# Kernel tuning notes

Measured on AMD Instinct MI355X. Metric: run time of the kernel, lower is better.

The kernel has to match this reference:

```python
import jax, jax.numpy as jnp
import numpy as np

PCH_SIZE = 8
STRIDE = 3


def setup_inputs() -> dict:
    key = jax.random.key(0)
    x = jax.random.normal(key, (8, 3, 512, 512), dtype=jnp.float32)
    return {"x": x}


def _estimate_noise(x, p=PCH_SIZE, s=STRIDE):
    B = x.shape[0]
    # Extract overlapping patches: [B, C*p*p, Hp, Wp] (NCHW input).
    pch = jax.lax.conv_general_dilated_patches(x, (p, p), (s, s), 'VALID')
    d = pch.shape[1]                       # C*p*p = 192
    pch = pch.reshape(B, d, -1)            # [B, d, num_pch]
    num_pch = pch.shape[-1]
    mu = pch.mean(axis=-1, keepdims=True)
    X = pch - mu
    # Patch covariance: [B, d, d]
    sigma_X = jnp.einsum('bdn,ben->bde', X, X) / num_pch
    sig = jnp.sort(jnp.linalg.eigvalsh(sigma_X), axis=-1)  # [B, d], ascending

    # Vectorized version of the original sequential threshold search.
    # Loop iteration ii = -1..-d uses prefix sig[..., :d+ii] of length L = d-1..0.
    ks = jnp.arange(d)
    L = d - 1 - ks                          # prefix lengths in original loop order
    csum = jnp.cumsum(sig, axis=-1)         # [B, d]
    prefix_sum = jnp.where(L > 0, csum[:, jnp.clip(L - 1, 0, d - 1)], 0.0)  # [B, d]
    tau = prefix_sum / jnp.maximum(L, 1).astype(sig.dtype)                  # [B, d]

    j = jnp.arange(d)
    in_prefix = j[None, :] < L[:, None]     # [K, d] membership of eig j in prefix k
    greater = (sig[:, None, :] > tau[:, :, None]) & in_prefix[None]
    less = (sig[:, None, :] < tau[:, :, None]) & in_prefix[None]
    valid = greater.sum(axis=-1) == less.sum(axis=-1)  # [B, K]

    # First valid iteration in loop order (mirrors the `found` flag).
    idx = jnp.argmax(valid, axis=-1)                    # [B]
    tau_sel = jnp.take_along_axis(tau, idx[:, None], axis=-1)[:, 0]
    return jnp.sqrt(tau_sel)                             # [B]


def reference(x):
    return _estimate_noise(x)
```

## Files before the change

kernel.cpp:

```cpp
#include <hip/hip_runtime.h>
#include <math.h>

#define NB 8
#define NC 3
#define PD 192
#define IMG 512
#define NP 169
#define NPATCH 28561
#define INV_N (1.0f/28561.0f)
#define KST 32

typedef float f4 __attribute__((ext_vector_type(4)));
typedef f4 f4u __attribute__((aligned(4)));
typedef __bf16 bf16x8 __attribute__((ext_vector_type(8)));
typedef float f32x4 __attribute__((ext_vector_type(4)));

__device__ __forceinline__ float rdlane(float v, int lane) {
  return __uint_as_float(__builtin_amdgcn_readlane(__float_as_uint(v), lane));
}

template<int CTRL, int RM, int BM>
__device__ __forceinline__ float dpp_add(float x) {
  int sh = __builtin_amdgcn_update_dpp(0, __float_as_int(x), CTRL, RM, BM, false);
  return x + __int_as_float(sh);
}
__device__ __forceinline__ float wave_sum(float x) {
  x = dpp_add<0x111, 0xF, 0xF>(x);
  x = dpp_add<0x112, 0xF, 0xF>(x);
  x = dpp_add<0x114, 0xF, 0xF>(x);
  x = dpp_add<0x118, 0xF, 0xF>(x);
  x = dpp_add<0x142, 0xA, 0xF>(x);
  x = dpp_add<0x143, 0xC, 0xF>(x);
  return rdlane(x, 63);
}
__device__ __forceinline__ float row16_sum(float x) {
  x = dpp_add<0x111, 0xF, 0xF>(x);
  x = dpp_add<0x112, 0xF, 0xF>(x);
  x = dpp_add<0x114, 0xF, 0xF>(x);
  x = dpp_add<0x118, 0xF, 0xF>(x);
  return rdlane(x, 15);
}

__device__ __forceinline__ unsigned bfh(float v) {
  unsigned u = __float_as_uint(v);
  return (u + 0x7FFFu + ((u >> 16) & 1u)) >> 16;
}

__global__ __launch_bounds__(256) void row_sums_k(const float* __restrict__ x,
                                                  float* __restrict__ S) {
  int bid = blockIdx.x;
  int b = bid / PD, d = bid - b * PD;
  int c = d >> 6, ii = (d >> 3) & 7, jj = d & 7;
  const float* img = x + ((size_t)(b * NC + c)) * (IMG * IMG);
  float part = 0.f;
  for (int p = threadIdx.x; p < NPATCH; p += 256) {
    int ph = p / NP;
    int pw = p - ph * NP;
    part += img[(3 * ph + ii) * IMG + 3 * pw + jj];
  }
  __shared__ float red[256];
  int t = threadIdx.x;
  red[t] = part; __syncthreads();
  for (int s = 128; s > 0; s >>= 1) { if (t < s) red[t] += red[t + s]; __syncthreads(); }
  if (t == 0) S[bid] = red[0];
}

__global__ __launch_bounds__(512) void cov_gemm_k(const float* __restrict__ x,
                                                  float* __restrict__ partial,
                                                  int CH, int chunkSize) {
  int chunk = blockIdx.x % CH;
  int b = blockIdx.x / CH;
  int p0 = chunk * chunkSize;
  int pcount = NPATCH - p0;
  if (pcount > chunkSize) pcount = chunkSize;
  if (pcount < 0) pcount = 0;
  int nkt = (pcount + KST - 1) / KST;
  int pend = p0 + pcount;

  __shared__ unsigned short hiT[PD * 40];
  __shared__ unsigned short loT[PD * 40];

  int t = threadIdx.x;
  int l = t & 63, w = t >> 6;
  int wr = w >> 2, wc = w & 3;
  int m0 = wr * 96, n0 = wc * 48;
  const float* imgb = x + (size_t)b * NC * IMG * IMG;

  f32x4 acc[6][3];
#pragma unroll
  for (int i = 0; i < 6; ++i)
#pragma unroll
    for (int j = 0; j < 3; ++j)
      acc[i][j] = (f32x4){0.f, 0.f, 0.f, 0.f};

  int krow = (l >> 4) << 3;
  int rsel = l & 15;

  for (int kt = 0; kt < nkt; ++kt) {
    int pbase = p0 + kt * KST;
#pragma unroll
    for (int s = 0; s < 6; ++s) {
      int idx = (s << 9) + t;
      int f = idx >> 4, p2 = idx & 15;
      int c = f >> 6, ii = (f >> 3) & 7, jj = f & 7;
      const float* imgc = imgb + (size_t)c * IMG * IMG;
      int P0 = pbase + (p2 << 1);
      float v0 = 0.f, v1 = 0.f;
      if (P0 < pend) { int ph = P0 / NP, pw = P0 - ph * NP; v0 = imgc[(3 * ph + ii) * IMG + 3 * pw + jj]; }
      if (P0 + 1 < pend) { int ph = (P0 + 1) / NP, pw = (P0 + 1) - ph * NP; v1 = imgc[(3 * ph + ii) * IMG + 3 * pw + jj]; }
      unsigned h0 = bfh(v0), h1 = bfh(v1);
      float r0 = v0 - __uint_as_float(h0 << 16);
      float r1 = v1 - __uint_as_float(h1 << 16);
      unsigned g0 = bfh(r0), g1 = bfh(r1);
      *(unsigned*)&hiT[f * 40 + (p2 << 1)] = h0 | (h1 << 16);
      *(unsigned*)&loT[f * 40 + (p2 << 1)] = g0 | (g1 << 16);
    }
    __syncthreads();

    bf16x8 ah[6], al[6], bh[3], bl[3];
#pragma unroll
    for (int i = 0; i < 6; ++i) {
      int row = m0 + i * 16 + rsel;
      ah[i] = *(const bf16x8*)&hiT[row * 40 + krow];
      al[i] = *(const bf16x8*)&loT[row * 40 + krow];
    }
#pragma unroll
    for (int j = 0; j < 3; ++j) {
      int row = n0 + j * 16 + rsel;
      bh[j] = *(const bf16x8*)&hiT[row * 40 + krow];
      bl[j] = *(const bf16x8*)&loT[row * 40 + krow];
    }
#pragma unroll
    for (int i = 0; i < 6; ++i)
#pragma unroll
      for (int j = 0; j < 3; ++j) {
        acc[i][j] = __builtin_amdgcn_mfma_f32_16x16x32_bf16(ah[i], bh[j], acc[i][j], 0, 0, 0);
        acc[i][j] = __builtin_amdgcn_mfma_f32_16x16x32_bf16(ah[i], bl[j], acc[i][j], 0, 0, 0);
        acc[i][j] = __builtin_amdgcn_mfma_f32_16x16x32_bf16(al[i], bh[j], acc[i][j], 0, 0, 0);
      }
    __syncthreads();
  }

  float* outp = partial + ((size_t)chunk * NB + b) * PD * PD;
#pragma unroll
  for (int i = 0; i < 6; ++i) {
    int rowb = m0 + i * 16 + ((l >> 4) << 2);
#pragma unroll
    for (int r = 0; r < 4; ++r)
#pragma unroll
      for (int j = 0; j < 3; ++j)
        outp[(size_t)(rowb + r) * PD + n0 + j * 16 + (l & 15)] = acc[i][j][r];
  }
}

__global__ __launch_bounds__(256) void reduce_fin_k(const float* __restrict__ partial,
                                                    const float* __restrict__ S,
                                                    float* __restrict__ G, int CH) {
  int e = blockIdx.x * 256 + threadIdx.x;
  const int tot = NB * PD * PD;
  if (e >= tot) return;
  int b = e / (PD * PD);
  int rem = e - b * PD * PD;
  int i = rem / PD, j = rem - i * PD;
  float s = 0.f;
  for (int c = 0; c < CH; ++c) s += partial[((size_t)c * NB + b) * PD * PD + rem];
  float mui = S[b * PD + i] * INV_N, muj = S[b * PD + j] * INV_N;
  G[e] = s * INV_N - mui * muj;
}

__global__ __launch_bounds__(768, 3) void eigen_k(const float* __restrict__ sigma,
                                                  float* __restrict__ out) {
  __shared__ float ppt[PD][20];
  __shared__ float vvg[2][PD];
  __shared__ float wvg[PD];
  __shared__ float red0[2];
  __shared__ float red2[16];
  __shared__ float dd[PD], ee[PD], e2[PD];
  __shared__ float sig[PD], csum[PD];
  __shared__ float grd[8];
  __shared__ float scanw[4];
  __shared__ int   redi[4];
  __shared__ int   cntb[4][PD];

  int b = blockIdx.x, t = threadIdx.x;
  int w = t >> 6, l = t & 63;
  int colbase = w << 4;
  const float* M = sigma + (size_t)b * PD * PD;

  f4 a[3][4];
#pragma unroll
  for (int rr = 0; rr < 3; ++rr) {
    const float* mp = M + (size_t)((rr << 6) + l) * PD + colbase;
#pragma unroll
    for (int cc = 0; cc < 4; ++cc)
      a[rr][cc] = *(const f4*)(mp + (cc << 2));
  }
  if (t >= 12 && t < 16) red2[t] = 0.f;

  auto extract = [&](int c, float* av) {
#pragma unroll
    for (int cc = 0; cc < 4; ++cc)
#pragma unroll
      for (int e = 0; e < 4; ++e)
        if (colbase + (cc << 2) + e == c) {
          av[0] = a[0][cc][e]; av[1] = a[1][cc][e]; av[2] = a[2][cc][e];
        }
  };

  auto prep_core = [&](int c, float av0, float av1, float av2) {
    int k1 = c + 1;
    float am0 = (l >= k1) ? av0 : 0.f;
    float am1 = (l + 64 >= k1) ? av1 : 0.f;
    float am2 = (l + 128 >= k1) ? av2 : 0.f;
    float sq = wave_sum(am0 * am0 + am1 * am1 + am2 * am2);
    int slot2 = k1 >> 6;
    float tmp = (slot2 == 0) ? av0 : (slot2 == 1) ? av1 : av2;
    float x0 = rdlane(tmp, k1 & 63);
    float nrm = __builtin_amdgcn_sqrtf(sq);
    float alpha = (x0 >= 0.f) ? -nrm : nrm;
    bool degen = (sq < 1e-32f);
    float beta = degen ? 0.f : __builtin_amdgcn_rcpf(sq - alpha * x0);
    if (l == 0) {
      red0[c & 1] = beta;
      ee[c] = degen ? x0 : alpha;
    }
    float head = x0 - alpha;
    vvg[c & 1][l]       = (l       < k1) ? 0.f : (l       == k1) ? head : am0;
    vvg[c & 1][l + 64]  = (l + 64  < k1) ? 0.f : (l + 64  == k1) ? head : am1;
    vvg[c & 1][l + 128] = (l + 128 < k1) ? 0.f : (l + 128 == k1) ? head : am2;
  };

  if (w == 0) {
    float av[3] = {0.f, 0.f, 0.f};
    extract(0, av);
    prep_core(0, av[0], av[1], av[2]);
  }
  __syncthreads();

  for (int k = 0; k < PD - 2; ++k) {
    int cur = k & 1;
    int k1 = k + 1;
    bool wact = (colbase + 15) >= k1;

    float vr[3] = {0.f, 0.f, 0.f};
    f4 sv4[4];

    if (wact) {
      vr[0] = vvg[cur][l]; vr[1] = vvg[cur][l + 64]; vr[2] = vvg[cur][l + 128];
#pragma unroll
      for (int cc = 0; cc < 4; ++cc)
        sv4[cc] = *(const f4*)&vvg[cur][colbase + (cc << 2)];
      float dp = 0.f;
#pragma unroll
      for (int rr = 0; rr < 3; ++rr) {
        if ((rr << 6) + 63 >= k1) {
          f4 s4 = sv4[0] * a[rr][0] + sv4[1] * a[rr][1]
                + sv4[2] * a[rr][2] + sv4[3] * a[rr][3];
          float s = (s4.x + s4.y) + (s4.z + s4.w);
          ppt[(rr << 6) + l][w] = s;
          dp += vr[rr] * s;
        }
      }
      float dpt = wave_sum(dp);
      if (l == 0) red2[w] = dpt;
    } else if (k1 == colbase + 16) {
      ppt[l][w] = 0.f; ppt[l + 64][w] = 0.f; ppt[l + 128][w] = 0.f;
      if (l == 0) red2[w] = 0.f;
    }
    __syncthreads();

    if (wact) {
      float rv = red2[l & 15];
      float vt = row16_sum(rv);
      float beta = red0[cur];
      float Kc = 0.5f * beta * beta * vt;
      float wr[3] = {0.f, 0.f, 0.f};
#pragma unroll
      for (int rr = 0; rr < 3; ++rr) {
        if ((rr << 6) + 63 >= k1) {
          int row = (rr << 6) + l;
          f4 q = *(const f4*)&ppt[row][0];
          f4 q1 = *(const f4*)&ppt[row][4];
          f4 q2 = *(const f4*)&ppt[row][8];
          q += q1 + q2;
          float p = (q.x + q.y) + (q.z + q.w);
          wr[rr] = (row >= k1) ? (beta * p - Kc * vr[rr]) : 0.f;
          wvg[row] = wr[rr];
        }
      }
      f4 sw4[4];
#pragma unroll
      for (int cc = 0; cc < 4; ++cc)
        sw4[cc] = *(const f4*)&wvg[colbase + (cc << 2)];
      int cn = k + 1;
      if (w == (cn >> 4)) {
        float av[3] = {0.f, 0.f, 0.f};
        extract(cn, av);
        float svv = vvg[cur][cn];
        float swv = wvg[cn];
#pragma unroll
        for (int rr = 0; rr < 3; ++rr) av[rr] -= vr[rr] * swv + wr[rr] * svv;
        prep_core(cn, av[0], av[1], av[2]);
      }
#pragma unroll
      for (int rr = 0; rr < 3; ++rr) {
        if ((rr << 6) + 63 >= k1) {
          float vrr = vr[rr], wrr = wr[rr];
#pragma unroll
          for (int cc = 0; cc < 4; ++cc)
            a[rr][cc] -= sw4[cc] * vrr + sv4[cc] * wrr;
        }
      }
    }
    __syncthreads();
  }

#pragma unroll
  for (int rr = 0; rr < 3; ++rr) {
    int row = (rr << 6) + l;
#pragma unroll
    for (int cc = 0; cc < 4; ++cc)
#pragma unroll
      for (int e = 0; e < 4; ++e)
        if (colbase + (cc << 2) + e == row) dd[row] = a[rr][cc][e];
  }
  __syncthreads();

  if (t < PD - 1) e2[t] = ee[t] * ee[t];

  float glo = 1e30f, ghi = -1e30f;
  if (t < PD) {
    float r = 0.f;
    if (t > 0) r += fabsf(ee[t - 1]);
    if (t < PD - 1) r += fabsf(ee[t]);
    glo = dd[t] - r;
    ghi = dd[t] + r;
  }
#pragma unroll
  for (int off = 32; off; off >>= 1) {
    glo = fminf(glo, __shfl_xor(glo, off, 64));
    ghi = fmaxf(ghi, __shfl_xor(ghi, off, 64));
  }
  if (l == 0 && w < 3) { grd[w] = glo; grd[4 + w] = ghi; }
  __syncthreads();
  float gl = fminf(grd[0], fminf(grd[1], grd[2]));
  float gh = fmaxf(grd[4], fmaxf(grd[5], grd[6]));
  float wid = gh - gl;
  gl -= 1e-3f * wid + 1e-20f;
  gh += 1e-3f * wid + 1e-20f;

  {
    int we3 = w - (w / 3) * 3;
    int sub = w / 3;
    int e = (we3 << 6) + l;
    float lo = gl, hi = gh;
    for (int round = 0; round < 8; ++round) {
      float width = hi - lo;
      float xm = lo + width * (0.2f * (float)(sub + 1));
      int cnt = 0;
      float q = 1.0f;
      for (int i = 0; i < PD; ++i) {
        float term = (i > 0) ? e2[i - 1] * __builtin_amdgcn_rcpf(q) : 0.0f;
        q = (dd[i] - xm) - term;
        cnt += (q < 0.f);
        float aq = fabsf(q);
        if (aq < 1e-30f) q = (q < 0.f) ? -1e-30f : 1e-30f;
      }
      cntb[sub][e] = cnt;
      __syncthreads();
      int c0 = cntb[0][e], c1 = cntb[1][e], c2 = cntb[2][e], c3 = cntb[3][e];
      float mA = lo + width * 0.2f, mB = lo + width * 0.4f;
      float mC = lo + width * 0.6f, mD = lo + width * 0.8f;
      float nl = lo, nh = hi;
      if (c0 <= e) nl = mA;
      if (c1 <= e) nl = mB;
      if (c2 <= e) nl = mC;
      if (c3 <= e) nl = mD;
      if (c3 > e) nh = mD;
      if (c2 > e) nh = mC;
      if (c1 > e) nh = mB;
      if (c0 > e) nh = mA;
      lo = nl; hi = nh;
      __syncthreads();
    }
    if (sub == 0) sig[e] = 0.5f * (lo + hi);
  }
  __syncthreads();

  {
    float x = (t < PD) ? sig[t] : 0.f;
    float scn = x;
#pragma unroll
    for (int off = 1; off < 64; off <<= 1) {
      float u = __shfl_up(scn, off, 64);
      if (l >= off) scn += u;
    }
    if (l == 63 && w < 3) scanw[w] = scn;
    __syncthreads();
    if (t < PD) {
      float base = 0.f;
      if (w >= 1) base += scanw[0];
      if (w >= 2) base += scanw[1];
      csum[t] = scn + base;
    }
  }
  __syncthreads();

  float tau = 0.f;
  int vk = 1 << 30;
  if (t < PD) {
    int L = PD - 1 - t;
    tau = (L > 0) ? csum[L - 1] / (float)L : 0.0f;
    int gt = 0, lt2 = 0;
    for (int j = 0; j < L; ++j) {
      float svv = sig[j];
      gt  += (svv > tau);
      lt2 += (svv < tau);
    }
    if (gt == lt2) vk = t;
  }
#pragma unroll
  for (int off = 32; off; off >>= 1) vk = min(vk, __shfl_xor(vk, off, 64));
  if (l == 0 && w < 3) redi[w] = vk;
  __syncthreads();
  if (t == 0) {
    int g = min(redi[0], min(redi[1], redi[2]));
    redi[3] = (g == (1 << 30)) ? 0 : g;
  }
  __syncthreads();
  if (t < PD && t == redi[3]) out[b] = sqrtf(fmaxf(tau, 0.f));
}

extern "C" void kernel_launch(void* const* d_in, const int* in_sizes, int n_in,
                              void* d_out, int out_size, void* d_ws, size_t ws_size,
                              hipStream_t stream) {
  const float* x = (const float*)d_in[0];
  float* out = (float*)d_out;

  size_t gElems = (size_t)NB * PD * PD;
  int CH = 32;
  while (CH > 1 && ws_size < ((size_t)CH + 1) * gElems * 4 + (size_t)NB * PD * 4)
    CH >>= 1;
  float* G = (float*)d_ws;
  float* partial = G + gElems;
  float* S = partial + (size_t)CH * gElems;
  int chunkSize = (NPATCH + CH - 1) / CH;

  row_sums_k<<<NB * PD, 256, 0, stream>>>(x, S);
  cov_gemm_k<<<NB * CH, 512, 0, stream>>>(x, partial, CH, chunkSize);
  reduce_fin_k<<<(int)((gElems + 255) / 256), 256, 0, stream>>>(partial, S, G, CH);
  eigen_k<<<NB, 768, 0, stream>>>(G, out);
}
```

Measured before the change: 485.9 us.

## Fuse patch mean sums into covariance GEMM and reduce LDS conflicts in eigen kernel

Drops the separate row_sums kernel, which re-read the whole image with strided gathers, and accumulates per-feature sums from values the covariance GEMM already loads. Per-chunk partial sums go through shared memory into a small buffer, and a tiny extra kernel combines them. The eigen kernel also swizzles the ppt column index so the LDS writes are spread across banks, and lets only one wave write each wvg entry instead of every wave writing it. The cost is an extra launch, more shared memory in the GEMM, and a little more workspace.

```diff
diff --git a/kernel.cpp b/kernel.cpp
--- a/kernel.cpp
+++ b/kernel.cpp
@@ -11,7 +11,6 @@
 #define KST 32
 
 typedef float f4 __attribute__((ext_vector_type(4)));
-typedef f4 f4u __attribute__((aligned(4)));
 typedef __bf16 bf16x8 __attribute__((ext_vector_type(8)));
 typedef float f32x4 __attribute__((ext_vector_type(4)));
 
@@ -46,27 +45,9 @@
   return (u + 0x7FFFu + ((u >> 16) & 1u)) >> 16;
 }
 
-__global__ __launch_bounds__(256) void row_sums_k(const float* __restrict__ x,
-                                                  float* __restrict__ S) {
-  int bid = blockIdx.x;
-  int b = bid / PD, d = bid - b * PD;
-  int c = d >> 6, ii = (d >> 3) & 7, jj = d & 7;
-  const float* img = x + ((size_t)(b * NC + c)) * (IMG * IMG);
-  float part = 0.f;
-  for (int p = threadIdx.x; p < NPATCH; p += 256) {
-    int ph = p / NP;
-    int pw = p - ph * NP;
-    part += img[(3 * ph + ii) * IMG + 3 * pw + jj];
-  }
-  __shared__ float red[256];
-  int t = threadIdx.x;
-  red[t] = part; __syncthreads();
-  for (int s = 128; s > 0; s >>= 1) { if (t < s) red[t] += red[t + s]; __syncthreads(); }
-  if (t == 0) S[bid] = red[0];
-}
-
 __global__ __launch_bounds__(512) void cov_gemm_k(const float* __restrict__ x,
                                                   float* __restrict__ partial,
+                                                  float* __restrict__ Spart,
                                                   int CH, int chunkSize) {
   int chunk = blockIdx.x % CH;
   int b = blockIdx.x / CH;
@@ -79,6 +60,7 @@
 
   __shared__ unsigned short hiT[PD * 40];
   __shared__ unsigned short loT[PD * 40];
+  __shared__ float sred[PD * 16];
 
   int t = threadIdx.x;
   int l = t & 63, w = t >> 6;
@@ -92,6 +74,8 @@
 #pragma unroll
     for (int j = 0; j < 3; ++j)
       acc[i][j] = (f32x4){0.f, 0.f, 0.f, 0.f};
+
+  float fsum[6] = {0.f, 0.f, 0.f, 0.f, 0.f, 0.f};
 
   int krow = (l >> 4) << 3;
   int rsel = l & 15;
@@ -108,6 +92,7 @@
       float v0 = 0.f, v1 = 0.f;
       if (P0 < pend) { int ph = P0 / NP, pw = P0 - ph * NP; v0 = imgc[(3 * ph + ii) * IMG + 3 * pw + jj]; }
       if (P0 + 1 < pend) { int ph = (P0 + 1) / NP, pw = (P0 + 1) - ph * NP; v1 = imgc[(3 * ph + ii) * IMG + 3 * pw + jj]; }
+      fsum[s] += v0 + v1;
       unsigned h0 = bfh(v0), h1 = bfh(v1);
       float r0 = v0 - __uint_as_float(h0 << 16);
       float r1 = v1 - __uint_as_float(h1 << 16);
@@ -141,6 +126,19 @@
     __syncthreads();
   }
 
+#pragma unroll
+  for (int s = 0; s < 6; ++s) {
+    int f = (t >> 4) + (s << 5);
+    sred[(f << 4) | (t & 15)] = fsum[s];
+  }
+  __syncthreads();
+  if (t < PD) {
+    float s = 0.f;
+#pragma unroll
+    for (int p2 = 0; p2 < 16; ++p2) s += sred[(t << 4) | p2];
+    Spart[((size_t)chunk * NB + b) * PD + t] = s;
+  }
+
   float* outp = partial + ((size_t)chunk * NB + b) * PD * PD;
 #pragma unroll
   for (int i = 0; i < 6; ++i) {
@@ -151,6 +149,14 @@
       for (int j = 0; j < 3; ++j)
         outp[(size_t)(rowb + r) * PD + n0 + j * 16 + (l & 15)] = acc[i][j][r];
   }
+}
+
+__global__ __launch_bounds__(192) void musum_k(const float* __restrict__ Spart,
+                                               float* __restrict__ S, int CH) {
+  int b = blockIdx.x, t = threadIdx.x;
+  float s = 0.f;
+  for (int c = 0; c < CH; ++c) s += Spart[((size_t)c * NB + b) * PD + t];
+  S[b * PD + t] = s;
 }
 
 __global__ __launch_bounds__(256) void reduce_fin_k(const float* __restrict__ partial,
@@ -196,6 +202,9 @@
       a[rr][cc] = *(const f4*)(mp + (cc << 2));
   }
   if (t >= 12 && t < 16) red2[t] = 0.f;
+
+  int swc = w + (l >> 3);
+  if (swc >= 12) swc -= 12;
 
   auto extract = [&](int c, float* av) {
 #pragma unroll
@@ -257,14 +266,14 @@
           f4 s4 = sv4[0] * a[rr][0] + sv4[1] * a[rr][1]
                 + sv4[2] * a[rr][2] + sv4[3] * a[rr][3];
           float s = (s4.x + s4.y) + (s4.z + s4.w);
-          ppt[(rr << 6) + l][w] = s;
+          ppt[(rr << 6) + l][swc] = s;
           dp += vr[rr] * s;
         }
       }
       float dpt = wave_sum(dp);
       if (l == 0) red2[w] = dpt;
     } else if (k1 == colbase + 16) {
-      ppt[l][w] = 0.f; ppt[l + 64][w] = 0.f; ppt[l + 128][w] = 0.f;
+      ppt[l][swc] = 0.f; ppt[l + 64][swc] = 0.f; ppt[l + 128][swc] = 0.f;
       if (l == 0) red2[w] = 0.f;
     }
     __syncthreads();
@@ -285,7 +294,10 @@
           q += q1 + q2;
           float p = (q.x + q.y) + (q.z + q.w);
           wr[rr] = (row >= k1) ? (beta * p - Kc * vr[rr]) : 0.f;
-          wvg[row] = wr[rr];
+          if (rr == (w >> 2)) {
+            if ((l >> 4) == (w & 3))
+              wvg[row] = wr[rr];
+          }
         }
       }
       f4 sw4[4];
@@ -439,15 +451,18 @@
 
   size_t gElems = (size_t)NB * PD * PD;
   int CH = 32;
-  while (CH > 1 && ws_size < ((size_t)CH + 1) * gElems * 4 + (size_t)NB * PD * 4)
+  while (CH > 1 &&
+         ws_size < ((size_t)CH + 1) * gElems * 4 + (size_t)NB * PD * 4 +
+                   (size_t)CH * NB * PD * 4)
     CH >>= 1;
   float* G = (float*)d_ws;
   float* partial = G + gElems;
   float* S = partial + (size_t)CH * gElems;
+  float* Spart = S + (size_t)NB * PD;
   int chunkSize = (NPATCH + CH - 1) / CH;
 
-  row_sums_k<<<NB * PD, 256, 0, stream>>>(x, S);
-  cov_gemm_k<<<NB * CH, 512, 0, stream>>>(x, partial, CH, chunkSize);
+  cov_gemm_k<<<NB * CH, 512, 0, stream>>>(x, partial, Spart, CH, chunkSize);
+  musum_k<<<NB, 192, 0, stream>>>(Spart, S, CH);
   reduce_fin_k<<<(int)((gElems + 255) / 256), 256, 0, stream>>>(partial, S, G, CH);
   eigen_k<<<NB, 768, 0, stream>>>(G, out);
 }
```

Result: faster. 459.3 us (-5.5%).
